# Performance work log

Measured on AMD Instinct MI355X. Metric: run time of the kernel, lower is better.

The kernel has to match this reference:

```python
import jax, jax.numpy as jnp
import numpy as np

B, N, H = 128, 1024, 128          # graphs, nodes per graph, hidden size
K1, K2, K3 = 512, 256, 128        # ceil(ratio^l * N), ratio = 0.5
DEG = 8                           # avg degree
E = B * N * DEG                   # total edges (fixed, masked after pooling)


def gcn_conv(x, row, col, mask, W, b, n):
    h = x @ W
    deg = jax.ops.segment_sum(mask, col, num_segments=n) + 1.0  # + self loop
    dinv = jax.lax.rsqrt(deg)
    coef = (dinv[row] * dinv[col] * mask)[:, None]
    agg = jax.ops.segment_sum(h[row] * coef, col, num_segments=n)
    return agg + h * (dinv * dinv)[:, None] + b  # self-loop term + bias


def topk_pool(x, row, col, mask, p, n_graphs, n_per, k):
    # PyG TopKPooling: y = x.p/||p||, keep per-graph top-k, x' = x[perm]*tanh(y[perm])
    score = (x @ p) / jnp.linalg.norm(p)
    vals, idx = jax.lax.top_k(score.reshape(n_graphs, n_per), k)  # [B, k]
    sel = (idx + (jnp.arange(n_graphs) * n_per)[:, None]).reshape(-1)
    xs = x[sel] * jnp.tanh(vals.reshape(-1))[:, None]
    # relabel edges; drop edges touching removed nodes via mask
    newid = jnp.full((n_graphs * n_per,), -1, jnp.int32).at[sel].set(
        jnp.arange(n_graphs * k, dtype=jnp.int32))
    nr, nc = newid[row], newid[col]
    nmask = mask * ((nr >= 0) & (nc >= 0)).astype(mask.dtype)
    return xs, jnp.maximum(nr, 0), jnp.maximum(nc, 0), nmask


def readout(x, n_graphs, k):
    # cat([gmp, gap]) with contiguous equal-size graphs
    xg = x.reshape(n_graphs, k, -1)
    return jnp.concatenate([xg.max(axis=1), xg.mean(axis=1)], axis=1)


def _forward(x, edge_row, edge_col, W1, b1, p1, W2, b2, p2, W3, b3, p3):
    mask = jnp.ones((E,), x.dtype)
    h = jax.nn.relu(gcn_conv(x, edge_row, edge_col, mask, W1, b1, B * N))
    x1, r, c, m = topk_pool(h, edge_row, edge_col, mask, p1, B, N, K1)
    out = readout(x1, B, K1)
    h = jax.nn.relu(gcn_conv(x1, r, c, m, W2, b2, B * K1))
    x2, r, c, m = topk_pool(h, r, c, m, p2, B, K1, K2)
    out = out + readout(x2, B, K2)
    h = jax.nn.relu(gcn_conv(x2, r, c, m, W3, b3, B * K2))
    x3, r, c, m = topk_pool(h, r, c, m, p3, B, K2, K3)
    out = out + readout(x3, B, K3)
    return out  # [B, 2*H]


def setup_inputs() -> dict:
    key = jax.random.key(0)
    ks = jax.random.split(key, 12)
    x = jax.random.normal(ks[0], (B * N, H), jnp.float32)
    off = (jnp.arange(B, dtype=jnp.int32) * N)[:, None]
    edge_row = (jax.random.randint(ks[1], (B, N * DEG), 0, N, jnp.int32) + off).reshape(-1)
    edge_col = (jax.random.randint(ks[2], (B, N * DEG), 0, N, jnp.int32) + off).reshape(-1)
    s = 1.0 / np.sqrt(H)
    params = {}
    for i, tag in enumerate(["1", "2", "3"]):
        params["W" + tag] = jax.random.normal(ks[3 + 3 * i], (H, H), jnp.float32) * s
        params["b" + tag] = jnp.zeros((H,), jnp.float32)
        params["p" + tag] = jax.random.normal(ks[4 + 3 * i], (H,), jnp.float32)
    return {"x": x, "edge_row": edge_row, "edge_col": edge_col, **params}


def reference(x, edge_row, edge_col, W1, b1, p1, W2, b2, p2, W3, b3, p3):
    return _forward(x, edge_row, edge_col, W1, b1, p1, W2, b2, p2, W3, b3, p3)
```

## Files before the change

kernel.cpp:

```cpp
#include <hip/hip_runtime.h>
#include <math.h>

#define BG   128
#define NPER 1024
#define HDIM 128
#define NEDGE (BG * NPER * 8)
#define NMAX (BG * NPER)
#define EPG  (NEDGE / BG)
#define CAP  48
#define PRE  16
#define CROWS 64

typedef __attribute__((ext_vector_type(8))) short s16x8;
typedef __attribute__((ext_vector_type(4))) float f32x4;

static __device__ __forceinline__ ushort f2bf(float f) {
  uint u = __float_as_uint(f);
  return (ushort)((u + 0x7fffu + ((u >> 16) & 1u)) >> 16);
}
static __device__ __forceinline__ float bf2f(ushort h) {
  return __uint_as_float(((uint)h) << 16);
}


__global__ __launch_bounds__(256) void countfill_kernel(
    const int* __restrict__ cr, const int* __restrict__ cc,
    int* __restrict__ cnt, int* __restrict__ meta8,
    int* __restrict__ srcext, int mask) {
  int e = blockIdx.x * 256 + threadIdx.x;
  int c = cc[e];
  int rl = cr[e] & mask;
  int pos = atomicAdd(&cnt[c], 1);
  if (pos < PRE) {
    meta8[(size_t)c * PRE + pos] = rl;
  } else if (pos < CAP) {
    srcext[(size_t)c * CAP + pos] = rl;
  }
}

extern __shared__ float ldsbuf[];


__global__ __launch_bounds__(1024) void agg_lds_kernel(
    const float* __restrict__ x, float* __restrict__ z,
    const int* __restrict__ meta8, const int* __restrict__ srcext,
    const int* __restrict__ deg, int npg) {
  float* sX = ldsbuf;
  float* sDinv = sX + npg * 32;
  int g = blockIdx.x >> 2;
  int chunk = blockIdx.x & 3;
  int t = threadIdx.x;
  int base = g * npg;

  const float4* x4 = (const float4*)x;
  float4* sX4 = (float4*)sX;
  for (int i = t; i < npg * 8; i += 1024) {
    int r = i >> 3, l8 = i & 7;
    float dv = rsqrtf((float)deg[base + r] + 1.0f);
    float4 v = x4[(size_t)(base + r) * 32 + chunk * 8 + l8];
    v.x *= dv; v.y *= dv; v.z *= dv; v.w *= dv;
    sX4[i] = v;
  }
  for (int i = t; i < npg; i += 1024)
    sDinv[i] = rsqrtf((float)deg[base + i] + 1.0f);

  int dl = t >> 3, l = t & 7;
  const int4* m4 = (const int4*)meta8;
  float4* z4 = (float4*)z;

  int4 c0 = m4[(size_t)(base + dl) * 4 + 0];
  int4 c1 = m4[(size_t)(base + dl) * 4 + 1];
  int4 c2 = m4[(size_t)(base + dl) * 4 + 2];
  int4 c3 = m4[(size_t)(base + dl) * 4 + 3];
  int cdg = deg[base + dl];

  __syncthreads();

  for (int dst = dl; dst < npg; dst += 128) {
    int nxt = dst + 128;
    bool more = nxt < npg;
    int4 n0 = c0, n1 = c1, n2 = c2, n3 = c3;
    int ndg = cdg;
    if (more) {
      n0 = m4[(size_t)(base + nxt) * 4 + 0];
      n1 = m4[(size_t)(base + nxt) * 4 + 1];
      n2 = m4[(size_t)(base + nxt) * 4 + 2];
      n3 = m4[(size_t)(base + nxt) * 4 + 3];
      ndg = deg[base + nxt];
    }

    int node = base + dst;
    int d = cdg > CAP ? CAP : cdg;
    int dp = d > PRE ? PRE : d;
    float dc = sDinv[dst];

    int sA0 = (0 < dp) ? c0.x : dst;
    int sA1 = (1 < dp) ? c0.y : dst;
    int sA2 = (2 < dp) ? c0.z : dst;
    int sA3 = (3 < dp) ? c0.w : dst;
    int sA4 = (4 < dp) ? c1.x : dst;
    int sA5 = (5 < dp) ? c1.y : dst;
    int sA6 = (6 < dp) ? c1.z : dst;
    int sA7 = (7 < dp) ? c1.w : dst;
    float4 w  = sX4[dst * 8 + l];
    float4 p0 = sX4[sA0 * 8 + l];
    float4 p1 = sX4[sA1 * 8 + l];
    float4 p2 = sX4[sA2 * 8 + l];
    float4 p3 = sX4[sA3 * 8 + l];
    float4 p4 = sX4[sA4 * 8 + l];
    float4 p5 = sX4[sA5 * 8 + l];
    float4 p6 = sX4[sA6 * 8 + l];
    float4 p7 = sX4[sA7 * 8 + l];
    float4 a0, a1, a2, a3;
    a0.x = w.x + p0.x; a0.y = w.y + p0.y; a0.z = w.z + p0.z; a0.w = w.w + p0.w;
    a1.x = p1.x + p5.x; a1.y = p1.y + p5.y; a1.z = p1.z + p5.z; a1.w = p1.w + p5.w;
    a2.x = p2.x + p6.x; a2.y = p2.y + p6.y; a2.z = p2.z + p6.z; a2.w = p2.w + p6.w;
    a3.x = p3.x + p7.x; a3.y = p3.y + p7.y; a3.z = p3.z + p7.z; a3.w = p3.w + p7.w;
    a0.x += p4.x; a0.y += p4.y; a0.z += p4.z; a0.w += p4.w;

    int sB0 = (8 < dp) ? c2.x : dst;
    int sB1 = (9 < dp) ? c2.y : dst;
    int sB2 = (10 < dp) ? c2.z : dst;
    int sB3 = (11 < dp) ? c2.w : dst;
    int sB4 = (12 < dp) ? c3.x : dst;
    int sB5 = (13 < dp) ? c3.y : dst;
    int sB6 = (14 < dp) ? c3.z : dst;
    int sB7 = (15 < dp) ? c3.w : dst;
    float4 q0 = sX4[sB0 * 8 + l];
    float4 q1 = sX4[sB1 * 8 + l];
    float4 q2 = sX4[sB2 * 8 + l];
    float4 q3 = sX4[sB3 * 8 + l];
    float4 q4 = sX4[sB4 * 8 + l];
    float4 q5 = sX4[sB5 * 8 + l];
    float4 q6 = sX4[sB6 * 8 + l];
    float4 q7 = sX4[sB7 * 8 + l];
    a0.x += q0.x; a0.y += q0.y; a0.z += q0.z; a0.w += q0.w;
    a1.x += q1.x; a1.y += q1.y; a1.z += q1.z; a1.w += q1.w;
    a2.x += q2.x; a2.y += q2.y; a2.z += q2.z; a2.w += q2.w;
    a3.x += q3.x; a3.y += q3.y; a3.z += q3.z; a3.w += q3.w;
    a0.x += q4.x; a0.y += q4.y; a0.z += q4.z; a0.w += q4.w;
    a1.x += q5.x; a1.y += q5.y; a1.z += q5.z; a1.w += q5.w;
    a2.x += q6.x; a2.y += q6.y; a2.z += q6.z; a2.w += q6.w;
    a3.x += q7.x; a3.y += q7.y; a3.z += q7.z; a3.w += q7.w;

    if (d > PRE) {
      for (int e2 = PRE; e2 < d; ++e2) {
        int rl = srcext[(size_t)node * CAP + e2];
        float4 v0 = sX4[rl * 8 + l];
        a0.x += v0.x; a0.y += v0.y; a0.z += v0.z; a0.w += v0.w;
      }
    }

    float corr = (float)(PRE - dp);
    float4 o;
    o.x = (a0.x + a1.x + a2.x + a3.x - corr * w.x) * dc;
    o.y = (a0.y + a1.y + a2.y + a3.y - corr * w.y) * dc;
    o.z = (a0.z + a1.z + a2.z + a3.z - corr * w.z) * dc;
    o.w = (a0.w + a1.w + a2.w + a3.w - corr * w.w) * dc;
    z4[(size_t)node * 32 + chunk * 8 + l] = o;

    c0 = n0; c1 = n1; c2 = n2; c3 = n3; cdg = ndg;
  }
}


__global__ __launch_bounds__(256) void wsplit_kernel(
    const float* __restrict__ W0, const float* __restrict__ W1,
    const float* __restrict__ W2, ushort* __restrict__ wpk) {
  int id = blockIdx.x * 256 + threadIdx.x;
  int L = id >> 14;
  int r = id & 16383;
  int i = r & 7;
  int lane = (r >> 3) & 63;
  int nt = (r >> 9) & 7;
  int kt = (r >> 12) & 3;
  int k = kt * 32 + (lane >> 4) * 8 + i;
  int n = nt * 16 + (lane & 15);
  const float* W = (L == 0) ? W0 : (L == 1) ? W1 : W2;
  float v = W[k * HDIM + n];
  ushort h = f2bf(v);
  float r1 = v - bf2f(h);
  ushort m = f2bf(r1);
  ushort lo = f2bf(r1 - bf2f(m));
  size_t base = (size_t)L * 3 * 16384 + (size_t)r;
  wpk[base] = h;
  wpk[base + 16384] = m;
  wpk[base + 32768] = lo;
}


__global__ __launch_bounds__(256) void conv_mfma_kernel(
    float* __restrict__ zh, const ushort* __restrict__ wpk,
    const float* __restrict__ bias, const float* __restrict__ p,
    float* __restrict__ score) {
  int t = threadIdx.x;
  int wv = t >> 6, l = t & 63;
  int lr = l & 15, lq = l >> 4;
  int arow = blockIdx.x * CROWS + wv * 16 + lr;
  const float* zrow = zh + (size_t)arow * HDIM + lq * 8;

  s16x8 ah[4], am[4], al[4];
  #pragma unroll
  for (int kt = 0; kt < 4; ++kt) {
    float4 v0 = ((const float4*)(zrow + kt * 32))[0];
    float4 v1 = ((const float4*)(zrow + kt * 32))[1];
    float f[8] = {v0.x, v0.y, v0.z, v0.w, v1.x, v1.y, v1.z, v1.w};
    #pragma unroll
    for (int i = 0; i < 8; ++i) {
      ushort h = f2bf(f[i]);
      float r1 = f[i] - bf2f(h);
      ushort m = f2bf(r1);
      ushort lo = f2bf(r1 - bf2f(m));
      ah[kt][i] = (short)h; am[kt][i] = (short)m; al[kt][i] = (short)lo;
    }
  }

  f32x4 acc[8];
  #pragma unroll
  for (int nt = 0; nt < 8; ++nt) acc[nt] = (f32x4)(0.f);

  const s16x8* wh = (const s16x8*)wpk;
  const s16x8* wm = wh + 2048;
  const s16x8* wl = wm + 2048;

  #pragma unroll
  for (int kt = 0; kt < 4; ++kt) {
    #pragma unroll
    for (int nt = 0; nt < 8; ++nt) {
      int fi = (kt * 8 + nt) * 64 + l;
      s16x8 bh = wh[fi];
      s16x8 bm = wm[fi];
      s16x8 bl = wl[fi];
      acc[nt] = __builtin_amdgcn_mfma_f32_16x16x32_bf16(ah[kt], bh, acc[nt], 0, 0, 0);
      acc[nt] = __builtin_amdgcn_mfma_f32_16x16x32_bf16(ah[kt], bm, acc[nt], 0, 0, 0);
      acc[nt] = __builtin_amdgcn_mfma_f32_16x16x32_bf16(am[kt], bh, acc[nt], 0, 0, 0);
      acc[nt] = __builtin_amdgcn_mfma_f32_16x16x32_bf16(ah[kt], bl, acc[nt], 0, 0, 0);
      acc[nt] = __builtin_amdgcn_mfma_f32_16x16x32_bf16(al[kt], bh, acc[nt], 0, 0, 0);
      acc[nt] = __builtin_amdgcn_mfma_f32_16x16x32_bf16(am[kt], bm, acc[nt], 0, 0, 0);
    }
  }

  int orow = blockIdx.x * CROWS + wv * 16 + lq * 4;
  float part[4] = {0.f, 0.f, 0.f, 0.f};
  #pragma unroll
  for (int nt = 0; nt < 8; ++nt) {
    float bv = bias[nt * 16 + lr];
    float pv = p[nt * 16 + lr];
    #pragma unroll
    for (int j = 0; j < 4; ++j) {
      float hv = fmaxf(acc[nt][j] + bv, 0.f);
      part[j] += hv * pv;
      zh[(size_t)(orow + j) * HDIM + nt * 16 + lr] = hv;
    }
  }
  #pragma unroll
  for (int j = 0; j < 4; ++j) {
    #pragma unroll
    for (int s = 1; s < 16; s <<= 1) part[j] += __shfl_xor(part[j], s);
    if (lr == 0) score[orow + j] = part[j];
  }
}


__global__ __launch_bounds__(1024) void topk_mega_kernel(
    const float* __restrict__ score, const float* __restrict__ p,
    const float* __restrict__ h, float* __restrict__ xo,
    const int* __restrict__ in_r, const int* __restrict__ in_c,
    int* __restrict__ out_r, int* __restrict__ out_c,
    int* __restrict__ meta8, int* __restrict__ srcext,
    int* __restrict__ cnt, float* __restrict__ acc,
    float* __restrict__ outf, int P, int K, int L) {
  __shared__ float sv[1024];
  __shared__ int si[1024];
  __shared__ int snew[1024];
  __shared__ int scnt[512];
  __shared__ float s_pn;
  __shared__ float4 smx[32][32], ssm[32][32];
  int g = blockIdx.x;
  int t = threadIdx.x;

  if (L < 2 && t < 512) scnt[t] = 0;
  snew[t] = -1;
  if (t < 128) { float v = p[t]; sv[t] = v * v; }
  __syncthreads();
  for (int off = 64; off; off >>= 1) {
    if (t < off) sv[t] += sv[t + off];
    __syncthreads();
  }
  if (t == 0) s_pn = sqrtf(sv[0]);
  __syncthreads();
  float pn = s_pn;

  sv[t] = score[(size_t)g * P + t];
  si[t] = t;
  for (int size = 2; size <= P; size <<= 1) {
    for (int stride = size >> 1; stride; stride >>= 1) {
      __syncthreads();
      int j = t ^ stride;
      if (j > t) {
        float a = sv[t], b = sv[j];
        int ia = si[t], ib = si[j];
        bool tFirst = (a > b) || (a == b && ia < ib);
        bool up = ((t & size) == 0);
        if (up ? !tFirst : tFirst) {
          sv[t] = b; sv[j] = a;
          si[t] = ib; si[j] = ia;
        }
      }
    }
  }
  __syncthreads();
  if (t < K) {
    snew[si[t]] = t;
    sv[t] = tanhf(sv[t] / pn);
  }
  __syncthreads();

  int lane = t & 31, grp = t >> 5;
  const float4* h4 = (const float4*)h;
  float4* xo4 = (float4*)xo;
  size_t hbase = (size_t)g * P * 32;
  float4 mx = make_float4(-INFINITY, -INFINITY, -INFINITY, -INFINITY);
  float4 sm = make_float4(0.f, 0.f, 0.f, 0.f);
  #pragma unroll
  for (int i = 0; i < 16; ++i) {
    int j = grp * 16 + i;
    float th = sv[j];
    float4 v = h4[hbase + (size_t)si[j] * 32 + lane];
    v.x *= th; v.y *= th; v.z *= th; v.w *= th;
    xo4[((size_t)g * K + j) * 32 + lane] = v;
    mx.x = fmaxf(mx.x, v.x); mx.y = fmaxf(mx.y, v.y);
    mx.z = fmaxf(mx.z, v.z); mx.w = fmaxf(mx.w, v.w);
    sm.x += v.x; sm.y += v.y; sm.z += v.z; sm.w += v.w;
  }
  smx[grp][lane] = mx;
  ssm[grp][lane] = sm;
  __syncthreads();
  int ngrp = P >> 5;
  if (grp == 0) {
    for (int s2 = 1; s2 < ngrp; ++s2) {
      float4 m2 = smx[s2][lane], s3 = ssm[s2][lane];
      mx.x = fmaxf(mx.x, m2.x); mx.y = fmaxf(mx.y, m2.y);
      mx.z = fmaxf(mx.z, m2.z); mx.w = fmaxf(mx.w, m2.w);
      sm.x += s3.x; sm.y += s3.y; sm.z += s3.z; sm.w += s3.w;
    }
    int c0 = lane * 4;
    if (L < 2) {
      float* amax = acc + (size_t)L * BG * 256 + (size_t)g * 256;
      float* asum = amax + 128;
      amax[c0 + 0] = mx.x; amax[c0 + 1] = mx.y;
      amax[c0 + 2] = mx.z; amax[c0 + 3] = mx.w;
      asum[c0 + 0] = sm.x; asum[c0 + 1] = sm.y;
      asum[c0 + 2] = sm.z; asum[c0 + 3] = sm.w;
    } else {
      sv[c0 + 0] = mx.x; sv[c0 + 1] = mx.y;
      sv[c0 + 2] = mx.z; sv[c0 + 3] = mx.w;
      sv[128 + c0 + 0] = sm.x; sv[128 + c0 + 1] = sm.y;
      sv[128 + c0 + 2] = sm.z; sv[128 + c0 + 3] = sm.w;
    }
  }

  if (L == 2) {
    __syncthreads();
    float v;
    const float* a0 = acc + (size_t)g * 256;
    const float* a1 = acc + (size_t)BG * 256 + (size_t)g * 256;
    if (t < 128) {
      v = a0[t] + a1[t] + sv[t];
    } else {
      v = a0[t] * (1.f / 512.f) + a1[t] * (1.f / 256.f) + sv[t] * (1.f / 128.f);
    }
    outf[g * 256 + t] = v;
    return;
  }

  int ept = EPG / P;
  int ebase = g * EPG;
  for (int i = 0; i < ept; ++i) {
    int e = ebase + i * P + t;
    int r = in_r[e];
    int nr = -1, nc = -1;
    if (r >= 0) {
      nr = snew[r & (P - 1)];
      nc = snew[in_c[e] & (P - 1)];
    }
    bool ok = (nr >= 0) && (nc >= 0);
    out_r[e] = ok ? g * K + nr : -1;
    out_c[e] = ok ? g * K + nc : -1;
    if (ok) {
      int pos = atomicAdd(&scnt[nc], 1);
      size_t gnode = (size_t)g * K + nc;
      if (pos < PRE) {
        meta8[gnode * PRE + pos] = nr;
      } else if (pos < CAP) {
        srcext[gnode * CAP + pos] = nr;
      }
    }
  }
  __syncthreads();
  if (t < K) cnt[g * K + t] = scnt[t];
}


extern "C" void kernel_launch(void* const* d_in, const int* in_sizes, int n_in,
                              void* d_out, int out_size, void* d_ws, size_t ws_size,
                              hipStream_t stream) {
  const float* x0 = (const float*)d_in[0];
  const int* erow = (const int*)d_in[1];
  const int* ecol = (const int*)d_in[2];
  const float* Wm[3] = {(const float*)d_in[3], (const float*)d_in[6], (const float*)d_in[9]};
  const float* bm[3] = {(const float*)d_in[4], (const float*)d_in[7], (const float*)d_in[10]};
  const float* pm[3] = {(const float*)d_in[5], (const float*)d_in[8], (const float*)d_in[11]};

  char* w = (char*)d_ws;
  size_t off = 0;
  auto alloc = [&](size_t bytes) -> void* {
    void* ptr = w + off;
    off = (off + bytes + 255) & ~(size_t)255;
    return ptr;
  };
  int* cur_row = (int*)alloc((size_t)NEDGE * 4);
  int* cur_col = (int*)alloc((size_t)NEDGE * 4);
  int* meta8   = (int*)alloc((size_t)NMAX * PRE * 4);
  int* srcext  = (int*)alloc((size_t)NMAX * CAP * 4);
  int* cnt     = (int*)alloc((size_t)NMAX * 4);
  float* score = (float*)alloc((size_t)NMAX * 4);
  float* acc   = (float*)alloc((size_t)2 * BG * 256 * 4);
  float* zh    = (float*)alloc((size_t)NMAX * HDIM * 4);
  float* x1    = (float*)alloc((size_t)BG * 512 * HDIM * 4);
  float* x2    = (float*)alloc((size_t)BG * 256 * HDIM * 4);
  float* x3    = (float*)alloc((size_t)BG * 128 * HDIM * 4);
  ushort* wpk  = (ushort*)alloc((size_t)3 * 3 * 16384 * 2);

  hipFuncSetAttribute((const void*)agg_lds_kernel,
                      hipFuncAttributeMaxDynamicSharedMemorySize, 152 * 1024);

  hipMemsetAsync(cnt, 0, (size_t)NMAX * 4, stream);
  countfill_kernel<<<NEDGE / 256, 256, 0, stream>>>(erow, ecol, cnt, meta8,
                                                    srcext, NPER - 1);
  wsplit_kernel<<<(3 * 16384) / 256, 256, 0, stream>>>(Wm[0], Wm[1], Wm[2], wpk);

  const float* xin = x0;
  float* xout[3] = {x1, x2, x3};
  int Ps[3] = {1024, 512, 256};

  for (int L = 0; L < 3; ++L) {
    int P = Ps[L];
    int K = P >> 1;
    int n = BG * P;
    const int* in_r = (L == 0) ? erow : cur_row;
    const int* in_c = (L == 0) ? ecol : cur_col;
    size_t ldsBytes = (size_t)(P * 33) * 4;

    agg_lds_kernel<<<BG * 4, 1024, ldsBytes, stream>>>(
        xin, zh, meta8, srcext, cnt, P);
    conv_mfma_kernel<<<n / CROWS, 256, 0, stream>>>(
        zh, wpk + (size_t)L * 3 * 16384, bm[L], pm[L], score);
    topk_mega_kernel<<<BG, P, 0, stream>>>(
        score, pm[L], zh, xout[L], in_r, in_c, cur_row, cur_col,
        meta8, srcext, cnt, acc, (float*)d_out, P, K, L);
    xin = xout[L];
  }
}
```

Before: 377.0 us.

## Bucket nodes by degree to skip unused gather slots; double rows per MFMA block

Adds a degree-bucketing pass, run as a separate kernel for layer 1 and at the end of topk_mega for later layers. It orders nodes so low-degree (<=8) nodes come first, letting agg_lds_kernel skip the second group of 8 neighbor gathers and metadata loads for most warps with little divergence. Separately, conv_mfma_kernel now handles 128 rows per block (two row tiles per wave) so each B-fragment load is reused twice, with launch bounds raised to 2. The cost is an extra kernel, extra index indirection and more register pressure in the MFMA kernel.

```diff
diff --git a/kernel.cpp b/kernel.cpp
--- a/kernel.cpp
+++ b/kernel.cpp
@@ -9,7 +9,6 @@
 #define EPG  (NEDGE / BG)
 #define CAP  48
 #define PRE  16
-#define CROWS 64
 
 typedef __attribute__((ext_vector_type(8))) short s16x8;
 typedef __attribute__((ext_vector_type(4))) float f32x4;
@@ -38,13 +37,31 @@
   }
 }
 
+
+__global__ __launch_bounds__(1024) void degorder_kernel(
+    const int* __restrict__ cnt, int* __restrict__ order,
+    int* __restrict__ odeg) {
+  __shared__ int bb[2];
+  int g = blockIdx.x, t = threadIdx.x;
+  if (t < 2) bb[t] = 0;
+  __syncthreads();
+  int d = cnt[g * NPER + t];
+  int bkt = d > 8 ? 1 : 0;
+  int pos = atomicAdd(&bb[bkt], 1);
+  __syncthreads();
+  int slot = bkt ? bb[0] + pos : pos;
+  order[g * NPER + slot] = t;
+  odeg[g * NPER + slot] = d;
+}
+
 extern __shared__ float ldsbuf[];
 
 
 __global__ __launch_bounds__(1024) void agg_lds_kernel(
     const float* __restrict__ x, float* __restrict__ z,
     const int* __restrict__ meta8, const int* __restrict__ srcext,
-    const int* __restrict__ deg, int npg) {
+    const int* __restrict__ deg, const int* __restrict__ order,
+    const int* __restrict__ odeg, int npg) {
   float* sX = ldsbuf;
   float* sDinv = sX + npg * 32;
   int g = blockIdx.x >> 2;
@@ -68,29 +85,39 @@
   const int4* m4 = (const int4*)meta8;
   float4* z4 = (float4*)z;
 
-  int4 c0 = m4[(size_t)(base + dl) * 4 + 0];
-  int4 c1 = m4[(size_t)(base + dl) * 4 + 1];
-  int4 c2 = m4[(size_t)(base + dl) * 4 + 2];
-  int4 c3 = m4[(size_t)(base + dl) * 4 + 3];
-  int cdg = deg[base + dl];
-
-  __syncthreads();
-
-  for (int dst = dl; dst < npg; dst += 128) {
-    int nxt = dst + 128;
-    bool more = nxt < npg;
-    int4 n0 = c0, n1 = c1, n2 = c2, n3 = c3;
-    int ndg = cdg;
-    if (more) {
-      n0 = m4[(size_t)(base + nxt) * 4 + 0];
-      n1 = m4[(size_t)(base + nxt) * 4 + 1];
-      n2 = m4[(size_t)(base + nxt) * 4 + 2];
-      n3 = m4[(size_t)(base + nxt) * 4 + 3];
-      ndg = deg[base + nxt];
-    }
-
+  int ordc = order[base + dl];
+  int dpc  = odeg[base + dl];
+  int ordn = order[base + dl + 128];
+  int dpn  = odeg[base + dl + 128];
+  int4 c0 = m4[(size_t)(base + ordc) * 4 + 0];
+  int4 c1 = m4[(size_t)(base + ordc) * 4 + 1];
+  int4 c2 = {0, 0, 0, 0}, c3 = {0, 0, 0, 0};
+  if (dpc > 8) {
+    c2 = m4[(size_t)(base + ordc) * 4 + 2];
+    c3 = m4[(size_t)(base + ordc) * 4 + 3];
+  }
+
+  __syncthreads();
+
+  for (int slot = dl; slot < npg; slot += 128) {
+    int ordn2 = ordn, dpn2 = dpn;
+    if (slot + 256 < npg) {
+      ordn2 = order[base + slot + 256];
+      dpn2  = odeg[base + slot + 256];
+    }
+    int4 n0 = {0,0,0,0}, n1 = {0,0,0,0}, n2 = {0,0,0,0}, n3 = {0,0,0,0};
+    if (slot + 128 < npg) {
+      n0 = m4[(size_t)(base + ordn) * 4 + 0];
+      n1 = m4[(size_t)(base + ordn) * 4 + 1];
+      if (dpn > 8) {
+        n2 = m4[(size_t)(base + ordn) * 4 + 2];
+        n3 = m4[(size_t)(base + ordn) * 4 + 3];
+      }
+    }
+
+    int dst = ordc;
     int node = base + dst;
-    int d = cdg > CAP ? CAP : cdg;
+    int d = dpc > CAP ? CAP : dpc;
     int dp = d > PRE ? PRE : d;
     float dc = sDinv[dst];
 
@@ -118,30 +145,34 @@
     a3.x = p3.x + p7.x; a3.y = p3.y + p7.y; a3.z = p3.z + p7.z; a3.w = p3.w + p7.w;
     a0.x += p4.x; a0.y += p4.y; a0.z += p4.z; a0.w += p4.w;
 
-    int sB0 = (8 < dp) ? c2.x : dst;
-    int sB1 = (9 < dp) ? c2.y : dst;
-    int sB2 = (10 < dp) ? c2.z : dst;
-    int sB3 = (11 < dp) ? c2.w : dst;
-    int sB4 = (12 < dp) ? c3.x : dst;
-    int sB5 = (13 < dp) ? c3.y : dst;
-    int sB6 = (14 < dp) ? c3.z : dst;
-    int sB7 = (15 < dp) ? c3.w : dst;
-    float4 q0 = sX4[sB0 * 8 + l];
-    float4 q1 = sX4[sB1 * 8 + l];
-    float4 q2 = sX4[sB2 * 8 + l];
-    float4 q3 = sX4[sB3 * 8 + l];
-    float4 q4 = sX4[sB4 * 8 + l];
-    float4 q5 = sX4[sB5 * 8 + l];
-    float4 q6 = sX4[sB6 * 8 + l];
-    float4 q7 = sX4[sB7 * 8 + l];
-    a0.x += q0.x; a0.y += q0.y; a0.z += q0.z; a0.w += q0.w;
-    a1.x += q1.x; a1.y += q1.y; a1.z += q1.z; a1.w += q1.w;
-    a2.x += q2.x; a2.y += q2.y; a2.z += q2.z; a2.w += q2.w;
-    a3.x += q3.x; a3.y += q3.y; a3.z += q3.z; a3.w += q3.w;
-    a0.x += q4.x; a0.y += q4.y; a0.z += q4.z; a0.w += q4.w;
-    a1.x += q5.x; a1.y += q5.y; a1.z += q5.z; a1.w += q5.w;
-    a2.x += q6.x; a2.y += q6.y; a2.z += q6.z; a2.w += q6.w;
-    a3.x += q7.x; a3.y += q7.y; a3.z += q7.z; a3.w += q7.w;
+    int nslots = 8;
+    if (dp > 8) {
+      int sB0 = (8 < dp)  ? c2.x : dst;
+      int sB1 = (9 < dp)  ? c2.y : dst;
+      int sB2 = (10 < dp) ? c2.z : dst;
+      int sB3 = (11 < dp) ? c2.w : dst;
+      int sB4 = (12 < dp) ? c3.x : dst;
+      int sB5 = (13 < dp) ? c3.y : dst;
+      int sB6 = (14 < dp) ? c3.z : dst;
+      int sB7 = (15 < dp) ? c3.w : dst;
+      float4 q0 = sX4[sB0 * 8 + l];
+      float4 q1 = sX4[sB1 * 8 + l];
+      float4 q2 = sX4[sB2 * 8 + l];
+      float4 q3 = sX4[sB3 * 8 + l];
+      float4 q4 = sX4[sB4 * 8 + l];
+      float4 q5 = sX4[sB5 * 8 + l];
+      float4 q6 = sX4[sB6 * 8 + l];
+      float4 q7 = sX4[sB7 * 8 + l];
+      a0.x += q0.x; a0.y += q0.y; a0.z += q0.z; a0.w += q0.w;
+      a1.x += q1.x; a1.y += q1.y; a1.z += q1.z; a1.w += q1.w;
+      a2.x += q2.x; a2.y += q2.y; a2.z += q2.z; a2.w += q2.w;
+      a3.x += q3.x; a3.y += q3.y; a3.z += q3.z; a3.w += q3.w;
+      a0.x += q4.x; a0.y += q4.y; a0.z += q4.z; a0.w += q4.w;
+      a1.x += q5.x; a1.y += q5.y; a1.z += q5.z; a1.w += q5.w;
+      a2.x += q6.x; a2.y += q6.y; a2.z += q6.z; a2.w += q6.w;
+      a3.x += q7.x; a3.y += q7.y; a3.z += q7.z; a3.w += q7.w;
+      nslots = 16;
+    }
 
     if (d > PRE) {
       for (int e2 = PRE; e2 < d; ++e2) {
@@ -151,7 +182,7 @@
       }
     }
 
-    float corr = (float)(PRE - dp);
+    float corr = (float)(nslots - dp);
     float4 o;
     o.x = (a0.x + a1.x + a2.x + a3.x - corr * w.x) * dc;
     o.y = (a0.y + a1.y + a2.y + a3.y - corr * w.y) * dc;
@@ -159,7 +190,8 @@
     o.w = (a0.w + a1.w + a2.w + a3.w - corr * w.w) * dc;
     z4[(size_t)node * 32 + chunk * 8 + l] = o;
 
-    c0 = n0; c1 = n1; c2 = n2; c3 = n3; cdg = ndg;
+    ordc = ordn; dpc = dpn; ordn = ordn2; dpn = dpn2;
+    c0 = n0; c1 = n1; c2 = n2; c3 = n3;
   }
 }
 
@@ -189,35 +221,45 @@
 }
 
 
-__global__ __launch_bounds__(256) void conv_mfma_kernel(
+__global__ __launch_bounds__(256, 2) void conv_mfma_kernel(
     float* __restrict__ zh, const ushort* __restrict__ wpk,
     const float* __restrict__ bias, const float* __restrict__ p,
     float* __restrict__ score) {
   int t = threadIdx.x;
   int wv = t >> 6, l = t & 63;
   int lr = l & 15, lq = l >> 4;
-  int arow = blockIdx.x * CROWS + wv * 16 + lr;
-  const float* zrow = zh + (size_t)arow * HDIM + lq * 8;
-
-  s16x8 ah[4], am[4], al[4];
+  int arowA = blockIdx.x * 128 + wv * 16 + lr;
+  int arowB = arowA + 64;
+  const float* zrowA = zh + (size_t)arowA * HDIM + lq * 8;
+  const float* zrowB = zh + (size_t)arowB * HDIM + lq * 8;
+
+  s16x8 ahA[4], amA[4], alA[4], ahB[4], amB[4], alB[4];
   #pragma unroll
   for (int kt = 0; kt < 4; ++kt) {
-    float4 v0 = ((const float4*)(zrow + kt * 32))[0];
-    float4 v1 = ((const float4*)(zrow + kt * 32))[1];
-    float f[8] = {v0.x, v0.y, v0.z, v0.w, v1.x, v1.y, v1.z, v1.w};
+    float4 v0 = ((const float4*)(zrowA + kt * 32))[0];
+    float4 v1 = ((const float4*)(zrowA + kt * 32))[1];
+    float fA[8] = {v0.x, v0.y, v0.z, v0.w, v1.x, v1.y, v1.z, v1.w};
+    float4 u0 = ((const float4*)(zrowB + kt * 32))[0];
+    float4 u1 = ((const float4*)(zrowB + kt * 32))[1];
+    float fB[8] = {u0.x, u0.y, u0.z, u0.w, u1.x, u1.y, u1.z, u1.w};
     #pragma unroll
     for (int i = 0; i < 8; ++i) {
-      ushort h = f2bf(f[i]);
-      float r1 = f[i] - bf2f(h);
+      ushort h = f2bf(fA[i]);
+      float r1 = fA[i] - bf2f(h);
       ushort m = f2bf(r1);
       ushort lo = f2bf(r1 - bf2f(m));
-      ah[kt][i] = (short)h; am[kt][i] = (short)m; al[kt][i] = (short)lo;
-    }
-  }
-
-  f32x4 acc[8];
+      ahA[kt][i] = (short)h; amA[kt][i] = (short)m; alA[kt][i] = (short)lo;
+      h = f2bf(fB[i]);
+      r1 = fB[i] - bf2f(h);
+      m = f2bf(r1);
+      lo = f2bf(r1 - bf2f(m));
+      ahB[kt][i] = (short)h; amB[kt][i] = (short)m; alB[kt][i] = (short)lo;
+    }
+  }
+
+  f32x4 accA[8], accB[8];
   #pragma unroll
-  for (int nt = 0; nt < 8; ++nt) acc[nt] = (f32x4)(0.f);
+  for (int nt = 0; nt < 8; ++nt) { accA[nt] = (f32x4)(0.f); accB[nt] = (f32x4)(0.f); }
 
   const s16x8* wh = (const s16x8*)wpk;
   const s16x8* wm = wh + 2048;
@@ -231,33 +273,50 @@
       s16x8 bh = wh[fi];
       s16x8 bm = wm[fi];
       s16x8 bl = wl[fi];
-      acc[nt] = __builtin_amdgcn_mfma_f32_16x16x32_bf16(ah[kt], bh, acc[nt], 0, 0, 0);
-      acc[nt] = __builtin_amdgcn_mfma_f32_16x16x32_bf16(ah[kt], bm, acc[nt], 0, 0, 0);
-      acc[nt] = __builtin_amdgcn_mfma_f32_16x16x32_bf16(am[kt], bh, acc[nt], 0, 0, 0);
-      acc[nt] = __builtin_amdgcn_mfma_f32_16x16x32_bf16(ah[kt], bl, acc[nt], 0, 0, 0);
-      acc[nt] = __builtin_amdgcn_mfma_f32_16x16x32_bf16(al[kt], bh, acc[nt], 0, 0, 0);
-      acc[nt] = __builtin_amdgcn_mfma_f32_16x16x32_bf16(am[kt], bm, acc[nt], 0, 0, 0);
-    }
-  }
-
-  int orow = blockIdx.x * CROWS + wv * 16 + lq * 4;
-  float part[4] = {0.f, 0.f, 0.f, 0.f};
+      accA[nt] = __builtin_amdgcn_mfma_f32_16x16x32_bf16(ahA[kt], bh, accA[nt], 0, 0, 0);
+      accA[nt] = __builtin_amdgcn_mfma_f32_16x16x32_bf16(ahA[kt], bm, accA[nt], 0, 0, 0);
+      accA[nt] = __builtin_amdgcn_mfma_f32_16x16x32_bf16(amA[kt], bh, accA[nt], 0, 0, 0);
+      accA[nt] = __builtin_amdgcn_mfma_f32_16x16x32_bf16(ahA[kt], bl, accA[nt], 0, 0, 0);
+      accA[nt] = __builtin_amdgcn_mfma_f32_16x16x32_bf16(alA[kt], bh, accA[nt], 0, 0, 0);
+      accA[nt] = __builtin_amdgcn_mfma_f32_16x16x32_bf16(amA[kt], bm, accA[nt], 0, 0, 0);
+      accB[nt] = __builtin_amdgcn_mfma_f32_16x16x32_bf16(ahB[kt], bh, accB[nt], 0, 0, 0);
+      accB[nt] = __builtin_amdgcn_mfma_f32_16x16x32_bf16(ahB[kt], bm, accB[nt], 0, 0, 0);
+      accB[nt] = __builtin_amdgcn_mfma_f32_16x16x32_bf16(amB[kt], bh, accB[nt], 0, 0, 0);
+      accB[nt] = __builtin_amdgcn_mfma_f32_16x16x32_bf16(ahB[kt], bl, accB[nt], 0, 0, 0);
+      accB[nt] = __builtin_amdgcn_mfma_f32_16x16x32_bf16(alB[kt], bh, accB[nt], 0, 0, 0);
+      accB[nt] = __builtin_amdgcn_mfma_f32_16x16x32_bf16(amB[kt], bm, accB[nt], 0, 0, 0);
+    }
+  }
+
+  int orowA = blockIdx.x * 128 + wv * 16 + lq * 4;
+  int orowB = orowA + 64;
+  float partA[4] = {0.f, 0.f, 0.f, 0.f};
+  float partB[4] = {0.f, 0.f, 0.f, 0.f};
   #pragma unroll
   for (int nt = 0; nt < 8; ++nt) {
     float bv = bias[nt * 16 + lr];
     float pv = p[nt * 16 + lr];
     #pragma unroll
     for (int j = 0; j < 4; ++j) {
-      float hv = fmaxf(acc[nt][j] + bv, 0.f);
-      part[j] += hv * pv;
-      zh[(size_t)(orow + j) * HDIM + nt * 16 + lr] = hv;
+      float hA = fmaxf(accA[nt][j] + bv, 0.f);
+      partA[j] += hA * pv;
+      zh[(size_t)(orowA + j) * HDIM + nt * 16 + lr] = hA;
+      float hB = fmaxf(accB[nt][j] + bv, 0.f);
+      partB[j] += hB * pv;
+      zh[(size_t)(orowB + j) * HDIM + nt * 16 + lr] = hB;
     }
   }
   #pragma unroll
   for (int j = 0; j < 4; ++j) {
     #pragma unroll
-    for (int s = 1; s < 16; s <<= 1) part[j] += __shfl_xor(part[j], s);
-    if (lr == 0) score[orow + j] = part[j];
+    for (int s = 1; s < 16; s <<= 1) {
+      partA[j] += __shfl_xor(partA[j], s);
+      partB[j] += __shfl_xor(partB[j], s);
+    }
+    if (lr == 0) {
+      score[orowA + j] = partA[j];
+      score[orowB + j] = partB[j];
+    }
   }
 }
 
@@ -269,17 +328,20 @@
     int* __restrict__ out_r, int* __restrict__ out_c,
     int* __restrict__ meta8, int* __restrict__ srcext,
     int* __restrict__ cnt, float* __restrict__ acc,
+    int* __restrict__ order, int* __restrict__ odeg,
     float* __restrict__ outf, int P, int K, int L) {
   __shared__ float sv[1024];
   __shared__ int si[1024];
   __shared__ int snew[1024];
   __shared__ int scnt[512];
+  __shared__ int bb[2];
   __shared__ float s_pn;
   __shared__ float4 smx[32][32], ssm[32][32];
   int g = blockIdx.x;
   int t = threadIdx.x;
 
   if (L < 2 && t < 512) scnt[t] = 0;
+  if (t < 2) bb[t] = 0;
   snew[t] = -1;
   if (t < 128) { float v = p[t]; sv[t] = v * v; }
   __syncthreads();
@@ -399,6 +461,19 @@
   }
   __syncthreads();
   if (t < K) cnt[g * K + t] = scnt[t];
+
+  int bkt = 0, bpos = 0, bdeg = 0;
+  if (t < K) {
+    bdeg = scnt[t];
+    bkt = bdeg > 8 ? 1 : 0;
+    bpos = atomicAdd(&bb[bkt], 1);
+  }
+  __syncthreads();
+  if (t < K) {
+    int slot = bkt ? bb[0] + bpos : bpos;
+    order[g * K + slot] = t;
+    odeg[g * K + slot] = bdeg;
+  }
 }
 
 
@@ -424,6 +499,8 @@
   int* meta8   = (int*)alloc((size_t)NMAX * PRE * 4);
   int* srcext  = (int*)alloc((size_t)NMAX * CAP * 4);
   int* cnt     = (int*)alloc((size_t)NMAX * 4);
+  int* order   = (int*)alloc((size_t)NMAX * 4);
+  int* odeg    = (int*)alloc((size_t)NMAX * 4);
   float* score = (float*)alloc((size_t)NMAX * 4);
   float* acc   = (float*)alloc((size_t)2 * BG * 256 * 4);
   float* zh    = (float*)alloc((size_t)NMAX * HDIM * 4);
@@ -439,6 +516,7 @@
   countfill_kernel<<<NEDGE / 256, 256, 0, stream>>>(erow, ecol, cnt, meta8,
                                                     srcext, NPER - 1);
   wsplit_kernel<<<(3 * 16384) / 256, 256, 0, stream>>>(Wm[0], Wm[1], Wm[2], wpk);
+  degorder_kernel<<<BG, 1024, 0, stream>>>(cnt, order, odeg);
 
   const float* xin = x0;
   float* xout[3] = {x1, x2, x3};
@@ -453,12 +531,12 @@
     size_t ldsBytes = (size_t)(P * 33) * 4;
 
     agg_lds_kernel<<<BG * 4, 1024, ldsBytes, stream>>>(
-        xin, zh, meta8, srcext, cnt, P);
-    conv_mfma_kernel<<<n / CROWS, 256, 0, stream>>>(
+        xin, zh, meta8, srcext, cnt, order, odeg, P);
+    conv_mfma_kernel<<<n / 128, 256, 0, stream>>>(
         zh, wpk + (size_t)L * 3 * 16384, bm[L], pm[L], score);
     topk_mega_kernel<<<BG, P, 0, stream>>>(
         score, pm[L], zh, xout[L], in_r, in_c, cur_row, cur_col,
-        meta8, srcext, cnt, acc, (float*)d_out, P, K, L);
+        meta8, srcext, cnt, acc, order, odeg, (float*)d_out, P, K, L);
     xin = xout[L];
   }
 }
```

Measured after the change: 369.4 us. 2.0% less time.
